# Kernel optimization log

Hardware: AMD Instinct MI355X
Metric: run time of the kernel (lower is better)

## Reference

```python
import jax, jax.numpy as jnp
import numpy as np

N_EMBD = 1024
N_HEADS = 16
HEAD_SIZE = N_EMBD // N_HEADS
BLOCK_SIZE = 2048


def setup_inputs() -> dict:
    key = jax.random.key(0)
    kx, kqkv, kout = jax.random.split(key, 3)
    x = jax.random.normal(kx, (4, 2048, N_EMBD), dtype=jnp.float32)
    # Dense kernels (keras stores [in, out]); no biases.
    w_qkv = jax.random.normal(kqkv, (N_EMBD, 3 * N_EMBD), dtype=jnp.float32) * 0.02
    w_out = jax.random.normal(kout, (N_EMBD, N_EMBD), dtype=jnp.float32) * 0.02
    return {"x": x, "w_qkv": w_qkv, "w_out": w_out}


def reference(x, w_qkv, w_out):
    B, T, C = x.shape
    qkv = x @ w_qkv                                   # [B,T,3C]
    q, k, v = jnp.split(qkv, 3, axis=-1)

    def split_heads(t):
        return t.reshape(B, T, N_HEADS, HEAD_SIZE).transpose(0, 2, 1, 3)  # [B,H,T,D]

    q, k, v = split_heads(q), split_heads(k), split_heads(v)
    scale = jnp.sqrt(jnp.asarray(HEAD_SIZE, jnp.float32))
    scores = jnp.einsum('bhqd,bhkd->bhqk', q, k) / scale  # [B,H,T,T]
    # additive causal mask: 0 on/below diagonal, -1e9 above
    mask = jnp.triu(jnp.full((T, T), -1e9, dtype=jnp.float32), k=1)
    scores = scores + mask
    weights = jax.nn.softmax(scores, axis=-1)
    out = jnp.einsum('bhqk,bhkd->bhqd', weights, v)       # [B,H,T,D]
    out = out.transpose(0, 2, 1, 3).reshape(B, T, C)
    return out @ w_out
```

## Files before the change

kernel.cpp:

```cpp
#include <hip/hip_runtime.h>
#include <stdint.h>

typedef unsigned short u16;
typedef __attribute__((ext_vector_type(8))) short short8;
typedef __attribute__((ext_vector_type(4))) float f32x4;
typedef __attribute__((ext_vector_type(4))) float float4v;
typedef __attribute__((ext_vector_type(2))) uint32_t u32x2;

typedef const __attribute__((address_space(1))) void gvoid_t;
typedef __attribute__((address_space(3))) void lvoid_t;

#define N_EMBD 1024
#define NH 16
#define DH 64
#define TSEQ 2048
#define BATCH 4

#define MFMA16 __builtin_amdgcn_mfma_f32_16x16x32_bf16

__device__ __forceinline__ u16 f32_to_bf16(float f) {
  uint32_t x = __builtin_bit_cast(uint32_t, f);
  x = (x + 0x7FFFu + ((x >> 16) & 1u)) >> 16;
  return (u16)x;
}

__device__ __forceinline__ uint32_t cvtpk(float lo, float hi) {
  uint32_t r;
  asm("v_cvt_pk_bf16_f32 %0, %1, %2" : "=v"(r) : "v"(lo), "v"(hi));
  return r;
}

__device__ __forceinline__ float exp2v(float x) { return __builtin_amdgcn_exp2f(x); }

__device__ __forceinline__ void gload_lds16(const void* g, void* l) {
  __builtin_amdgcn_global_load_lds((gvoid_t*)g, (lvoid_t*)l, 16, 0, 0);
}

__global__ void cvt_kernel(const float* __restrict__ in, u16* __restrict__ out, int n4) {
  int i = blockIdx.x * blockDim.x + threadIdx.x;
  if (i < n4) {
    float4v v = *(const float4v*)(in + (size_t)i * 4);
    u32x2 o;
    o[0] = cvtpk(v[0], v[1]);
    o[1] = cvtpk(v[2], v[3]);
    *(u32x2*)(out + (size_t)i * 4) = o;
  }
}

__global__ void transpose_bf16(const float* __restrict__ in, u16* __restrict__ out,
                               int R, int C) {
  __shared__ u16 tile[32][33];
  int r0 = blockIdx.x * 32, c0 = blockIdx.y * 32;
  int tx = threadIdx.x & 31, ty = threadIdx.x >> 5;
#pragma unroll
  for (int i = 0; i < 4; i++)
    tile[ty + i * 8][tx] = f32_to_bf16(in[(size_t)(r0 + ty + i * 8) * C + c0 + tx]);
  __syncthreads();
#pragma unroll
  for (int i = 0; i < 4; i++)
    out[(size_t)(c0 + ty + i * 8) * R + r0 + tx] = tile[tx][ty + i * 8];
}

template <int EPI>
__global__ __launch_bounds__(256)
void gemm128(const u16* __restrict__ A, const u16* __restrict__ Bt,
             float* __restrict__ Cf, u16* __restrict__ Qb, u16* __restrict__ Kb,
             u16* __restrict__ Vt, int M, int N, int K) {
  __shared__ u16 sA[128 * 64];
  __shared__ u16 sB[128 * 64];
  const int tid = threadIdx.x;
  const int lane = tid & 63, w = tid >> 6;
  const int wm = w >> 1, wn = w & 1;
  const int l15 = lane & 15, lg = lane >> 4;
  const int m0 = blockIdx.x * 128, n0 = blockIdx.y * 128;
  f32x4 acc[4][4] = {};
  const int srow = tid >> 3, scb = tid & 7;

  auto stage = [&](int k0) {
#pragma unroll
    for (int i = 0; i < 4; i++) {
      int row = i * 32 + srow;
      int cb = scb ^ (row & 7);
      gload_lds16(A + (size_t)(m0 + row) * K + k0 + cb * 8, sA + i * 2048 + w * 512);
      gload_lds16(Bt + (size_t)(n0 + row) * K + k0 + cb * 8, sB + i * 2048 + w * 512);
    }
  };

  stage(0);
  for (int k0 = 0; k0 < K; k0 += 64) {
    __syncthreads();
    short8 af[4][2], bf[4][2];
#pragma unroll
    for (int mi = 0; mi < 4; mi++)
#pragma unroll
      for (int kk = 0; kk < 2; kk++) {
        int ra = wm * 64 + mi * 16 + l15;
        af[mi][kk] = *(const short8*)(sA + ra * 64 + ((kk * 4 + lg) ^ (ra & 7)) * 8);
        int rb = wn * 64 + mi * 16 + l15;
        bf[mi][kk] = *(const short8*)(sB + rb * 64 + ((kk * 4 + lg) ^ (rb & 7)) * 8);
      }
    if (k0 + 64 < K) {
      __syncthreads();
      stage(k0 + 64);
    }
#pragma unroll
    for (int kk = 0; kk < 2; kk++)
#pragma unroll
      for (int mi = 0; mi < 4; mi++)
#pragma unroll
        for (int ni = 0; ni < 4; ni++)
          acc[mi][ni] = MFMA16(af[mi][kk], bf[ni][kk], acc[mi][ni], 0, 0, 0);
  }

#pragma unroll
  for (int mi = 0; mi < 4; mi++)
#pragma unroll
    for (int ni = 0; ni < 4; ni++) {
      const int mb = m0 + wm * 64 + mi * 16 + lg * 4;
      const int n = n0 + wn * 64 + ni * 16 + l15;
      if (EPI == 0) {
#pragma unroll
        for (int r = 0; r < 4; r++)
          Cf[(size_t)(mb + r) * N + n] = acc[mi][ni][r];
      } else {
        const int b = mb >> 11, t = mb & 2047;
        const int sec = n >> 10, c = n & 1023;
        const int h = c >> 6, d = c & 63;
        if (sec == 2) {
          u32x2 pkd;
          pkd[0] = cvtpk(acc[mi][ni][0], acc[mi][ni][1]);
          pkd[1] = cvtpk(acc[mi][ni][2], acc[mi][ni][3]);
          *(u32x2*)(Vt + ((size_t)(b * NH + h) * DH + d) * TSEQ + t) = pkd;
        } else {
          u16* dst = (sec == 0) ? Qb : Kb;
          const float sc = (sec == 0) ? 0.1803368801111204f : 1.0f;
#pragma unroll
          for (int r = 0; r < 4; r++)
            dst[((size_t)(b * NH + h) * TSEQ + t + r) * DH + d] = f32_to_bf16(acc[mi][ni][r] * sc);
        }
      }
    }
}

__global__ __launch_bounds__(256)
void attn_kernel(const u16* __restrict__ Q, const u16* __restrict__ K,
                 const u16* __restrict__ Vt, u16* __restrict__ AO) {
  __shared__ u16 sK[2][64 * 64];
  __shared__ u16 sV[2][64 * 64];
  __shared__ u16 sP[4][2][16 * 64];
  const int tid = threadIdx.x;
  const int lane = tid & 63, w = tid >> 6;
  const int l15 = lane & 15, lg = lane >> 4;
  const int id = blockIdx.x;
  const int qt = 15 - (id >> 6);
  const int bh = id & 63;
  const int qb0 = qt * 128;
  const size_t bh_off = (size_t)bh * TSEQ * DH;
  const int q0a = qb0 + w * 16;
  const int q0b = qb0 + 64 + w * 16;

  short8 bq[2][2];
#pragma unroll
  for (int qg = 0; qg < 2; qg++) {
    int q0 = qg ? q0b : q0a;
#pragma unroll
    for (int kk = 0; kk < 2; kk++)
      bq[qg][kk] = *(const short8*)(Q + bh_off + (size_t)(q0 + l15) * DH + kk * 32 + lg * 8);
  }

  f32x4 accO[2][4] = {};
  float mrow[2] = {-3e38f, -3e38f};
  float lrow[2] = {0.f, 0.f};

  const int srow = tid >> 3, scb = tid & 7;

  auto stage = [&](int it, int buf) {
    const int k0 = it * 64;
    u16* dK = sK[buf];
    u16* dV = sV[buf];
#pragma unroll
    for (int i = 0; i < 2; i++) {
      int r = i * 32 + srow;
      int cb = scb ^ (r & 7);
      gload_lds16(K + bh_off + (size_t)(k0 + r) * DH + cb * 8, dK + i * 2048 + w * 512);
      gload_lds16(Vt + bh_off + (size_t)r * TSEQ + k0 + cb * 8, dV + i * 2048 + w * 512);
    }
  };

  const int ntiles = 2 * qt + 2;
  stage(0, 0);
  for (int it = 0; it < ntiles; ++it) {
    const int k0 = it * 64;
    __syncthreads();
    const int cur = it & 1;
    if (it + 1 < ntiles) stage(it + 1, cur ^ 1);
    if (k0 > q0b + 15) continue;

    const u16* cK = sK[cur];
    const u16* cV = sV[cur];

    short8 ak[4][2];
#pragma unroll
    for (int kb = 0; kb < 4; kb++)
#pragma unroll
      for (int kk = 0; kk < 2; kk++) {
        int rk = kb * 16 + l15;
        ak[kb][kk] = *(const short8*)(cK + rk * 64 + (((kk * 4 + lg) ^ (rk & 7)) * 8));
      }

#pragma unroll
    for (int qg = 0; qg < 2; qg++) {
      const int q0 = qg ? q0b : q0a;
      if (k0 <= q0 + 15) {
        f32x4 accST[4] = {};
        __builtin_amdgcn_s_setprio(1);
#pragma unroll
        for (int kk = 0; kk < 2; kk++)
#pragma unroll
          for (int kb = 0; kb < 4; kb++)
            accST[kb] = MFMA16(ak[kb][kk], bq[qg][kk], accST[kb], 0, 0, 0);
        __builtin_amdgcn_s_setprio(0);

        if (k0 + 63 > q0) {
#pragma unroll
          for (int kb = 0; kb < 4; kb++)
#pragma unroll
            for (int r = 0; r < 4; r++)
              if (k0 + kb * 16 + lg * 4 + r > q0 + l15) accST[kb][r] = -1e30f;
        }

        float t0 = fmaxf(fmaxf(accST[0][0], accST[0][1]), fmaxf(accST[0][2], accST[0][3]));
        float t1 = fmaxf(fmaxf(accST[1][0], accST[1][1]), fmaxf(accST[1][2], accST[1][3]));
        float t2 = fmaxf(fmaxf(accST[2][0], accST[2][1]), fmaxf(accST[2][2], accST[2][3]));
        float t3 = fmaxf(fmaxf(accST[3][0], accST[3][1]), fmaxf(accST[3][2], accST[3][3]));
        float mt = fmaxf(fmaxf(t0, t1), fmaxf(t2, t3));
        mt = fmaxf(mt, __shfl_xor(mt, 16));
        mt = fmaxf(mt, __shfl_xor(mt, 32));

        const float mold = mrow[qg];
        float mnew = mold;
        if (!__all(mt <= mold + 8.0f)) {
          mnew = fmaxf(mold, mt);
          const float alpha = exp2v(mold - mnew);
          mrow[qg] = mnew;
          lrow[qg] *= alpha;
#pragma unroll
          for (int di = 0; di < 4; di++)
#pragma unroll
            for (int j = 0; j < 4; j++) accO[qg][di][j] *= alpha;
        }

        uint32_t* sPq = (uint32_t*)sP[w][qg];
        const int sw = l15 & 7;
        float rsum = 0.f;
#pragma unroll
        for (int kb = 0; kb < 4; kb++) {
          float p0 = exp2v(accST[kb][0] - mnew);
          float p1 = exp2v(accST[kb][1] - mnew);
          float p2 = exp2v(accST[kb][2] - mnew);
          float p3 = exp2v(accST[kb][3] - mnew);
          rsum += (p0 + p1) + (p2 + p3);
          int off32 = l15 * 32 + ((((kb * 2 + (lg >> 1)) ^ sw) << 2) | ((lg & 1) << 1));
          uint32_t* dst = sPq + off32;
          dst[0] = cvtpk(p0, p1);
          dst[1] = cvtpk(p2, p3);
        }
        rsum += __shfl_xor(rsum, 16);
        rsum += __shfl_xor(rsum, 32);
        lrow[qg] += rsum;
      }
    }

    asm volatile("s_waitcnt lgkmcnt(0)" ::: "memory");

    short8 bv[2][4];
#pragma unroll
    for (int kk = 0; kk < 2; kk++)
#pragma unroll
      for (int di = 0; di < 4; di++) {
        int rv = di * 16 + l15;
        bv[kk][di] = *(const short8*)(cV + rv * 64 + (((kk * 4 + lg) ^ (rv & 7)) * 8));
      }
#pragma unroll
    for (int qg = 0; qg < 2; qg++) {
      const int q0 = qg ? q0b : q0a;
      if (k0 <= q0 + 15) {
        const u16* sPq = sP[w][qg];
        short8 ap[2];
#pragma unroll
        for (int kk = 0; kk < 2; kk++)
          ap[kk] = *(const short8*)(sPq + l15 * 64 + (((kk * 4 + lg) ^ (l15 & 7)) * 8));
        __builtin_amdgcn_s_setprio(1);
#pragma unroll
        for (int kk = 0; kk < 2; kk++)
#pragma unroll
          for (int db = 0; db < 4; db++)
            accO[qg][db] = MFMA16(bv[kk][db], ap[kk], accO[qg][db], 0, 0, 0);
        __builtin_amdgcn_s_setprio(0);
      }
    }
  }

  const int b = bh >> 4, h = bh & 15;
#pragma unroll
  for (int qg = 0; qg < 2; qg++) {
    const int q0 = qg ? q0b : q0a;
    const int t = q0 + l15;
    const float inv = 1.0f / lrow[qg];
    u16* orow = AO + ((size_t)b * TSEQ + t) * N_EMBD + h * 64 + lg * 4;
#pragma unroll
    for (int db = 0; db < 4; db++) {
      u32x2 pkd;
      pkd[0] = cvtpk(accO[qg][db][0] * inv, accO[qg][db][1] * inv);
      pkd[1] = cvtpk(accO[qg][db][2] * inv, accO[qg][db][3] * inv);
      *(u32x2*)(orow + db * 16) = pkd;
    }
  }
}

extern "C" void kernel_launch(void* const* d_in, const int* in_sizes, int n_in,
                              void* d_out, int out_size, void* d_ws, size_t ws_size,
                              hipStream_t stream) {
  const float* x = (const float*)d_in[0];
  const float* w_qkv = (const float*)d_in[1];
  const float* w_out = (const float*)d_in[2];
  float* out = (float*)d_out;
  char* ws = (char*)d_ws;
  const size_t MB = 1 << 20;
  u16* xb    = (u16*)(ws);
  u16* wqkvT = (u16*)(ws + 16 * MB);
  u16* woutT = (u16*)(ws + 22 * MB);
  u16* Qb    = (u16*)(ws + 24 * MB);
  u16* Kb    = (u16*)(ws + 40 * MB);
  u16* Vt    = (u16*)(ws + 56 * MB);
  u16* AO    = xb;

  cvt_kernel<<<8192, 256, 0, stream>>>(x, xb, (BATCH * TSEQ * N_EMBD) / 4);
  transpose_bf16<<<dim3(32, 96, 1), 256, 0, stream>>>(w_qkv, wqkvT, 1024, 3072);
  transpose_bf16<<<dim3(32, 32, 1), 256, 0, stream>>>(w_out, woutT, 1024, 1024);
  gemm128<1><<<dim3(64, 24), 256, 0, stream>>>(xb, wqkvT, nullptr, Qb, Kb, Vt,
                                               BATCH * TSEQ, 3 * N_EMBD, N_EMBD);
  attn_kernel<<<1024, 256, 0, stream>>>(Qb, Kb, Vt, AO);
  gemm128<0><<<dim3(64, 8), 256, 0, stream>>>(AO, woutT, out, nullptr, nullptr, nullptr,
                                              BATCH * TSEQ, N_EMBD, N_EMBD);
}
```

Before: 238.2 us.

## Switch attention to 32x32 MFMA and keep P in registers via lane shuffles

The attention kernel moves from 16x16x32 MFMA with two 16-row query groups per wave to 32x32x16 MFMA covering one 32-row query block per wave. The probability tile P is no longer written to and re-read from shared memory. Instead it is repacked in registers with cross-half-wave shuffles into the B-operand layout for the PV product. This is meant to remove LDS traffic and a waitcnt on P, and to use the larger MFMA shape for better operand reuse. The cost is higher accumulator register pressure and the loss of the finer per-16-row causal skipping.

```diff
diff --git a/kernel.cpp b/kernel.cpp
--- a/kernel.cpp
+++ b/kernel.cpp
@@ -4,8 +4,10 @@
 typedef unsigned short u16;
 typedef __attribute__((ext_vector_type(8))) short short8;
 typedef __attribute__((ext_vector_type(4))) float f32x4;
+typedef __attribute__((ext_vector_type(16))) float f32x16;
 typedef __attribute__((ext_vector_type(4))) float float4v;
 typedef __attribute__((ext_vector_type(2))) uint32_t u32x2;
+typedef __attribute__((ext_vector_type(4))) uint32_t u32x4;
 
 typedef const __attribute__((address_space(1))) void gvoid_t;
 typedef __attribute__((address_space(3))) void lvoid_t;
@@ -17,6 +19,7 @@
 #define BATCH 4
 
 #define MFMA16 __builtin_amdgcn_mfma_f32_16x16x32_bf16
+#define MFMA32 __builtin_amdgcn_mfma_f32_32x32x16_bf16
 
 __device__ __forceinline__ u16 f32_to_bf16(float f) {
   uint32_t x = __builtin_bit_cast(uint32_t, f);
@@ -147,30 +150,24 @@
                  const u16* __restrict__ Vt, u16* __restrict__ AO) {
   __shared__ u16 sK[2][64 * 64];
   __shared__ u16 sV[2][64 * 64];
-  __shared__ u16 sP[4][2][16 * 64];
   const int tid = threadIdx.x;
   const int lane = tid & 63, w = tid >> 6;
-  const int l15 = lane & 15, lg = lane >> 4;
+  const int l31 = lane & 31;
+  const int b5 = lane >> 5;
   const int id = blockIdx.x;
   const int qt = 15 - (id >> 6);
   const int bh = id & 63;
   const int qb0 = qt * 128;
   const size_t bh_off = (size_t)bh * TSEQ * DH;
-  const int q0a = qb0 + w * 16;
-  const int q0b = qb0 + 64 + w * 16;
-
-  short8 bq[2][2];
-#pragma unroll
-  for (int qg = 0; qg < 2; qg++) {
-    int q0 = qg ? q0b : q0a;
-#pragma unroll
-    for (int kk = 0; kk < 2; kk++)
-      bq[qg][kk] = *(const short8*)(Q + bh_off + (size_t)(q0 + l15) * DH + kk * 32 + lg * 8);
-  }
-
-  f32x4 accO[2][4] = {};
-  float mrow[2] = {-3e38f, -3e38f};
-  float lrow[2] = {0.f, 0.f};
+  const int q0 = qb0 + w * 32;
+
+  short8 bq[4];
+#pragma unroll
+  for (int ks = 0; ks < 4; ks++)
+    bq[ks] = *(const short8*)(Q + bh_off + (size_t)(q0 + l31) * DH + ks * 16 + b5 * 8);
+
+  f32x16 accO[2] = {};
+  float mrow = -3e38f, lrow = 0.f;
 
   const int srow = tid >> 3, scb = tid & 7;
 
@@ -194,128 +191,123 @@
     __syncthreads();
     const int cur = it & 1;
     if (it + 1 < ntiles) stage(it + 1, cur ^ 1);
-    if (k0 > q0b + 15) continue;
+    if (k0 > q0 + 31) continue;
 
     const u16* cK = sK[cur];
     const u16* cV = sV[cur];
 
-    short8 ak[4][2];
-#pragma unroll
-    for (int kb = 0; kb < 4; kb++)
-#pragma unroll
-      for (int kk = 0; kk < 2; kk++) {
-        int rk = kb * 16 + l15;
-        ak[kb][kk] = *(const short8*)(cK + rk * 64 + (((kk * 4 + lg) ^ (rk & 7)) * 8));
-      }
-
-#pragma unroll
-    for (int qg = 0; qg < 2; qg++) {
-      const int q0 = qg ? q0b : q0a;
-      if (k0 <= q0 + 15) {
-        f32x4 accST[4] = {};
-        __builtin_amdgcn_s_setprio(1);
-#pragma unroll
-        for (int kk = 0; kk < 2; kk++)
-#pragma unroll
-          for (int kb = 0; kb < 4; kb++)
-            accST[kb] = MFMA16(ak[kb][kk], bq[qg][kk], accST[kb], 0, 0, 0);
-        __builtin_amdgcn_s_setprio(0);
-
-        if (k0 + 63 > q0) {
-#pragma unroll
-          for (int kb = 0; kb < 4; kb++)
-#pragma unroll
-            for (int r = 0; r < 4; r++)
-              if (k0 + kb * 16 + lg * 4 + r > q0 + l15) accST[kb][r] = -1e30f;
+    short8 ak[2][4];
+#pragma unroll
+    for (int kb = 0; kb < 2; kb++)
+#pragma unroll
+      for (int ks = 0; ks < 4; ks++) {
+        int rk = kb * 32 + l31;
+        ak[kb][ks] = *(const short8*)(cK + rk * 64 + (((ks * 2 + b5) ^ (rk & 7)) * 8));
+      }
+
+    f32x16 accS[2] = {};
+    __builtin_amdgcn_s_setprio(1);
+#pragma unroll
+    for (int ks = 0; ks < 4; ks++)
+#pragma unroll
+      for (int kb = 0; kb < 2; kb++)
+        accS[kb] = MFMA32(ak[kb][ks], bq[ks], accS[kb], 0, 0, 0);
+    __builtin_amdgcn_s_setprio(0);
+
+    if (k0 + 63 > q0) {
+#pragma unroll
+      for (int kb = 0; kb < 2; kb++)
+#pragma unroll
+        for (int reg = 0; reg < 16; reg++) {
+          int kg = k0 + kb * 32 + (reg & 3) + 8 * (reg >> 2) + 4 * b5;
+          if (kg > q0 + l31) accS[kb][reg] = -1e30f;
         }
-
-        float t0 = fmaxf(fmaxf(accST[0][0], accST[0][1]), fmaxf(accST[0][2], accST[0][3]));
-        float t1 = fmaxf(fmaxf(accST[1][0], accST[1][1]), fmaxf(accST[1][2], accST[1][3]));
-        float t2 = fmaxf(fmaxf(accST[2][0], accST[2][1]), fmaxf(accST[2][2], accST[2][3]));
-        float t3 = fmaxf(fmaxf(accST[3][0], accST[3][1]), fmaxf(accST[3][2], accST[3][3]));
-        float mt = fmaxf(fmaxf(t0, t1), fmaxf(t2, t3));
-        mt = fmaxf(mt, __shfl_xor(mt, 16));
-        mt = fmaxf(mt, __shfl_xor(mt, 32));
-
-        const float mold = mrow[qg];
-        float mnew = mold;
-        if (!__all(mt <= mold + 8.0f)) {
-          mnew = fmaxf(mold, mt);
-          const float alpha = exp2v(mold - mnew);
-          mrow[qg] = mnew;
-          lrow[qg] *= alpha;
-#pragma unroll
-          for (int di = 0; di < 4; di++)
-#pragma unroll
-            for (int j = 0; j < 4; j++) accO[qg][di][j] *= alpha;
-        }
-
-        uint32_t* sPq = (uint32_t*)sP[w][qg];
-        const int sw = l15 & 7;
-        float rsum = 0.f;
-#pragma unroll
-        for (int kb = 0; kb < 4; kb++) {
-          float p0 = exp2v(accST[kb][0] - mnew);
-          float p1 = exp2v(accST[kb][1] - mnew);
-          float p2 = exp2v(accST[kb][2] - mnew);
-          float p3 = exp2v(accST[kb][3] - mnew);
-          rsum += (p0 + p1) + (p2 + p3);
-          int off32 = l15 * 32 + ((((kb * 2 + (lg >> 1)) ^ sw) << 2) | ((lg & 1) << 1));
-          uint32_t* dst = sPq + off32;
-          dst[0] = cvtpk(p0, p1);
-          dst[1] = cvtpk(p2, p3);
-        }
-        rsum += __shfl_xor(rsum, 16);
-        rsum += __shfl_xor(rsum, 32);
-        lrow[qg] += rsum;
-      }
-    }
-
-    asm volatile("s_waitcnt lgkmcnt(0)" ::: "memory");
-
-    short8 bv[2][4];
-#pragma unroll
-    for (int kk = 0; kk < 2; kk++)
-#pragma unroll
-      for (int di = 0; di < 4; di++) {
-        int rv = di * 16 + l15;
-        bv[kk][di] = *(const short8*)(cV + rv * 64 + (((kk * 4 + lg) ^ (rv & 7)) * 8));
-      }
-#pragma unroll
-    for (int qg = 0; qg < 2; qg++) {
-      const int q0 = qg ? q0b : q0a;
-      if (k0 <= q0 + 15) {
-        const u16* sPq = sP[w][qg];
-        short8 ap[2];
-#pragma unroll
-        for (int kk = 0; kk < 2; kk++)
-          ap[kk] = *(const short8*)(sPq + l15 * 64 + (((kk * 4 + lg) ^ (l15 & 7)) * 8));
-        __builtin_amdgcn_s_setprio(1);
-#pragma unroll
-        for (int kk = 0; kk < 2; kk++)
-#pragma unroll
-          for (int db = 0; db < 4; db++)
-            accO[qg][db] = MFMA16(bv[kk][db], ap[kk], accO[qg][db], 0, 0, 0);
-        __builtin_amdgcn_s_setprio(0);
-      }
-    }
+    }
+
+    float mt = fmaxf(accS[0][0], accS[0][1]);
+#pragma unroll
+    for (int reg = 2; reg < 16; reg++) mt = fmaxf(mt, accS[0][reg]);
+#pragma unroll
+    for (int reg = 0; reg < 16; reg++) mt = fmaxf(mt, accS[1][reg]);
+    mt = fmaxf(mt, __shfl_xor(mt, 32));
+
+    float mnew = mrow;
+    if (!__all(mt <= mrow + 8.0f)) {
+      mnew = fmaxf(mrow, mt);
+      const float alpha = exp2v(mrow - mnew);
+      mrow = mnew;
+      lrow *= alpha;
+#pragma unroll
+      for (int db = 0; db < 2; db++)
+#pragma unroll
+        for (int reg = 0; reg < 16; reg++) accO[db][reg] *= alpha;
+    }
+
+    uint32_t pk[2][4][2];
+    float rsum = 0.f;
+#pragma unroll
+    for (int kb = 0; kb < 2; kb++)
+#pragma unroll
+      for (int r1 = 0; r1 < 4; r1++) {
+        float p0 = exp2v(accS[kb][r1 * 4 + 0] - mnew);
+        float p1 = exp2v(accS[kb][r1 * 4 + 1] - mnew);
+        float p2 = exp2v(accS[kb][r1 * 4 + 2] - mnew);
+        float p3 = exp2v(accS[kb][r1 * 4 + 3] - mnew);
+        rsum += (p0 + p1) + (p2 + p3);
+        pk[kb][r1][0] = cvtpk(p0, p1);
+        pk[kb][r1][1] = cvtpk(p2, p3);
+      }
+    rsum += __shfl_xor(rsum, 32);
+    lrow += rsum;
+
+    short8 bp[4];
+#pragma unroll
+    for (int ks = 0; ks < 4; ks++) {
+      const int kb = ks >> 1, base = (ks & 1) * 2;
+      uint32_t A0 = b5 ? pk[kb][base + 1][0] : pk[kb][base][0];
+      uint32_t A1 = b5 ? pk[kb][base + 1][1] : pk[kb][base][1];
+      uint32_t B0 = b5 ? pk[kb][base][0] : pk[kb][base + 1][0];
+      uint32_t B1 = b5 ? pk[kb][base][1] : pk[kb][base + 1][1];
+      uint32_t Bs0 = __shfl_xor(B0, 32);
+      uint32_t Bs1 = __shfl_xor(B1, 32);
+      u32x4 v;
+      v[0] = b5 ? Bs0 : A0;
+      v[1] = b5 ? Bs1 : A1;
+      v[2] = b5 ? A0 : Bs0;
+      v[3] = b5 ? A1 : Bs1;
+      bp[ks] = __builtin_bit_cast(short8, v);
+    }
+
+    short8 av[2][4];
+#pragma unroll
+    for (int db = 0; db < 2; db++)
+#pragma unroll
+      for (int ks = 0; ks < 4; ks++) {
+        int rv = db * 32 + l31;
+        av[db][ks] = *(const short8*)(cV + rv * 64 + (((ks * 2 + b5) ^ (rv & 7)) * 8));
+      }
+    __builtin_amdgcn_s_setprio(1);
+#pragma unroll
+    for (int ks = 0; ks < 4; ks++)
+#pragma unroll
+      for (int db = 0; db < 2; db++)
+        accO[db] = MFMA32(av[db][ks], bp[ks], accO[db], 0, 0, 0);
+    __builtin_amdgcn_s_setprio(0);
   }
 
   const int b = bh >> 4, h = bh & 15;
-#pragma unroll
-  for (int qg = 0; qg < 2; qg++) {
-    const int q0 = qg ? q0b : q0a;
-    const int t = q0 + l15;
-    const float inv = 1.0f / lrow[qg];
-    u16* orow = AO + ((size_t)b * TSEQ + t) * N_EMBD + h * 64 + lg * 4;
-#pragma unroll
-    for (int db = 0; db < 4; db++) {
+  const int t = q0 + l31;
+  const float inv = 1.0f / lrow;
+  u16* orow = AO + ((size_t)b * TSEQ + t) * N_EMBD + h * 64 + 4 * b5;
+#pragma unroll
+  for (int db = 0; db < 2; db++)
+#pragma unroll
+    for (int r1 = 0; r1 < 4; r1++) {
       u32x2 pkd;
-      pkd[0] = cvtpk(accO[qg][db][0] * inv, accO[qg][db][1] * inv);
-      pkd[1] = cvtpk(accO[qg][db][2] * inv, accO[qg][db][3] * inv);
-      *(u32x2*)(orow + db * 16) = pkd;
-    }
-  }
+      pkd[0] = cvtpk(accO[db][r1 * 4 + 0] * inv, accO[db][r1 * 4 + 1] * inv);
+      pkd[1] = cvtpk(accO[db][r1 * 4 + 2] * inv, accO[db][r1 * 4 + 3] * inv);
+      *(u32x2*)(orow + db * 32 + r1 * 8) = pkd;
+    }
 }
 
 extern "C" void kernel_launch(void* const* d_in, const int* in_sizes, int n_in,
```

New measurement: 225.7 us. 1.06x faster.
